# Optimization experiments

Hardware: AMD Instinct MI355X
Metric: run time of the kernel (lower is better)

Reference implementation:

```python
import jax, jax.numpy as jnp
import numpy as np

B, T, C = 4, 2048, 768
NH, NKV, HD = 12, 12, 64
RMS_EPS = 1e-6


def rms_norm(x):
    return x * jax.lax.rsqrt(jnp.mean(x * x, axis=-1, keepdims=True) + RMS_EPS)


def apply_rotary_emb(x, cos, sin):
    # x: [B,T,H,D], cos/sin: [T,D/2]
    d2 = x.shape[-1] // 2
    x1, x2 = x[..., :d2], x[..., d2:]
    c = cos[None, :, None, :]
    s = sin[None, :, None, :]
    return jnp.concatenate([x1 * c - x2 * s, x1 * s + x2 * c], axis=-1)


def setup_inputs() -> dict:
    key = jax.random.key(0)
    ks = jax.random.split(key, 10)
    inv_freq = 1.0 / (100000.0 ** (np.arange(0, HD, 2, dtype=np.float32) / HD))  # [HD/2]
    t = np.arange(T, dtype=np.float32)
    freqs = np.outer(t, inv_freq)  # [T, HD/2]
    return {
        "x": jax.random.normal(ks[0], (B, T, C), jnp.float32),
        "ve": jax.random.normal(ks[1], (B, T, C), jnp.float32),
        "cos": jnp.asarray(np.cos(freqs)),
        "sin": jnp.asarray(np.sin(freqs)),
        "Wq": jax.random.normal(ks[2], (C, C), jnp.float32) * (1.0 / np.sqrt(C)),
        "Wk": jax.random.normal(ks[3], (C, C), jnp.float32) * (1.0 / np.sqrt(C)),
        "Wv": jax.random.normal(ks[4], (C, C), jnp.float32) * (1.0 / np.sqrt(C)),
        "Wproj": jax.random.normal(ks[5], (C, C), jnp.float32) * (1.0 / np.sqrt(C)),
        "Wgate": jax.random.normal(ks[6], (NKV, 12), jnp.float32) * 0.1,
        "window_left": 1024,
    }


def reference(x, ve, cos, sin, Wq, Wk, Wv, Wproj, Wgate, window_left):
    q = (x @ Wq.T).reshape(B, T, NH, HD)
    k = (x @ Wk.T).reshape(B, T, NKV, HD)
    v = (x @ Wv.T).reshape(B, T, NKV, HD)

    # value-embedding gating (has_ve path): gate = 3*sigmoid(Linear(x[...,:12]))
    ve_h = ve.reshape(B, T, NKV, HD)
    gate = 3.0 * jax.nn.sigmoid(x[..., :12] @ Wgate.T)  # [B,T,NKV]
    v = v + gate[..., None] * ve_h

    q = apply_rotary_emb(q, cos, sin)
    k = apply_rotary_emb(k, cos, sin)
    q = rms_norm(q) * 1.2
    k = rms_norm(k) * 1.2

    # sliding-window causal bias
    row = jnp.arange(T)[:, None]
    col = jnp.arange(T)[None, :]
    mask = (row >= col) & ((row - col) <= window_left)
    bias = jnp.where(mask, 0.0, -1e9).astype(x.dtype)  # [T,T]

    scale = 1.0 / np.sqrt(HD)
    att = jnp.einsum("bqhd,bkhd->bhqk", q, k) * scale + bias[None, None]
    att = jax.nn.softmax(att, axis=-1)
    y = jnp.einsum("bhqk,bkhd->bqhd", att, v).reshape(B, T, C)
    return y @ Wproj.T
```

## Files before the change

### kernel.cpp

```cpp
#include <hip/hip_runtime.h>
#include <hip/hip_bf16.h>
#include <cstdint>
#include <cstddef>

#define B_  4
#define T_  2048
#define C_  768
#define NH_ 12
#define HD_ 64

typedef __bf16 bf16_t;
typedef __attribute__((ext_vector_type(8))) __bf16 bf16x8;
typedef __attribute__((ext_vector_type(4))) __bf16 bf16x4;
typedef __attribute__((ext_vector_type(4))) float floatx4;
typedef __attribute__((ext_vector_type(8))) unsigned short ushort8;

#define MFMA16(a, b, c) __builtin_amdgcn_mfma_f32_16x16x32_bf16((a), (b), (c), 0, 0, 0)

#define SM_C1 0.18033688f
#define SM_C2 -17.3123405f

typedef const __attribute__((address_space(1))) uint8_t* gptr_t;
typedef __attribute__((address_space(3))) uint8_t* lptr_t;

static __device__ __forceinline__ void gld16(const void* g, void* l) {
    __builtin_amdgcn_global_load_lds((gptr_t)g, (lptr_t)l, 16, 0, 0);
}

static __device__ __forceinline__ float bfl(unsigned p) {
    return __builtin_bit_cast(float, p << 16);
}
static __device__ __forceinline__ float bfh(unsigned p) {
    return __builtin_bit_cast(float, p & 0xffff0000u);
}

__global__ __launch_bounds__(256) void cvt_all_kernel(
    const void* s0, const void* s1, const void* s2, const void* s3,
    const void* s4, const void* s5, const void* s6, const void* s7, const void* s8,
    bf16_t* d0, bf16_t* d1, bf16_t* d2, bf16_t* d3,
    bf16_t* d4, bf16_t* d5, bf16_t* d6, bf16_t* d7, bf16_t* d8)
{
    const bool isf32 = (((const unsigned short*)s2)[0] == 0);
    if (!isf32) return;
    const void* srcs[9] = {s0, s1, s2, s3, s4, s5, s6, s7, s8};
    bf16_t*     dsts[9] = {d0, d1, d2, d3, d4, d5, d6, d7, d8};
    const int   ns[9]   = {B_*T_*C_, B_*T_*C_, T_*32, T_*32,
                           C_*C_, C_*C_, C_*C_, C_*C_, 144};
    const int t = blockIdx.y;
    const float* sf = (const float*)srcs[t];
    bf16_t*     dst = dsts[t];
    const int   nc  = ns[t] >> 3;
    const int stride = gridDim.x * 256;
    for (int i = blockIdx.x * 256 + threadIdx.x; i < nc; i += stride) {
        ushort8 o;
#pragma unroll
        for (int j = 0; j < 8; j++)
            o[j] = (unsigned short)__builtin_bit_cast(unsigned short,
                     (bf16_t)sf[i * 8 + j]);
        *(ushort8*)&dst[i * 8] = o;
    }
}

__global__ __launch_bounds__(256) void gemm_qkv_fused(
    const void* xr,  const bf16_t* xc,
    const void* wqr, const bf16_t* wqc,
    const void* wkr, const bf16_t* wkc,
    const void* wvr, const bf16_t* wvc,
    const void* cr,  const bf16_t* ccv,
    const void* sr,  const bf16_t* scv,
    const void* ver, const bf16_t* vec,
    const void* wgr, const bf16_t* wgc,
    bf16_t* qn, bf16_t* kn, bf16_t* vt)
{
    __shared__ alignas(16) char sm[36864];
    const bool f32 = (((const unsigned short*)cr)[0] == 0);
    const bf16_t* X  = f32 ? xc  : (const bf16_t*)xr;
    const bf16_t* WQ = f32 ? wqc : (const bf16_t*)wqr;
    const bf16_t* WK = f32 ? wkc : (const bf16_t*)wkr;
    const bf16_t* WV = f32 ? wvc : (const bf16_t*)wvr;
    const bf16_t* CC = f32 ? ccv : (const bf16_t*)cr;
    const bf16_t* SS = f32 ? scv : (const bf16_t*)sr;
    const bf16_t* VE = f32 ? vec : (const bf16_t*)ver;
    const bf16_t* WG = f32 ? wgc : (const bf16_t*)wgr;

    const int sel = blockIdx.y / 6;
    const int nt  = blockIdx.y % 6;
    const int m0  = blockIdx.x * 128;
    const int n0  = nt * 128;
    const bf16_t* Bm = (sel == 0) ? WQ : (sel == 1) ? WK : WV;

    bf16_t* As = (bf16_t*)sm;
    bf16_t* Bs = (bf16_t*)(sm + 16384);

    const int tid  = threadIdx.x;
    const int lane = tid & 63;
    const int wid  = tid >> 6;
    const int m16  = lane & 15;
    const int quad = lane >> 4;
    const int wm   = (wid >> 1) * 64;
    const int wn   = (wid & 1) * 64;
    const int srow = lane >> 2;
    const int soct = (lane & 3) * 8;

    floatx4 acc[4][4];
#pragma unroll
    for (int i = 0; i < 4; i++)
#pragma unroll
        for (int j = 0; j < 4; j++) acc[i][j] = (floatx4){0.f, 0.f, 0.f, 0.f};

    for (int k0 = 0; k0 < C_; k0 += 64) {
        const bf16_t* ga0 = &X[(size_t)(m0 + 16 * wid + srow) * C_ + k0 + soct];
        const bf16_t* gb0 = &Bm[(size_t)(n0 + 16 * wid + srow) * C_ + k0 + soct];
        gld16(ga0,                        As + wid * 512);
        gld16(ga0 + (size_t)64 * C_,      As + wid * 512 + 2048);
        gld16(gb0,                        Bs + wid * 512);
        gld16(gb0 + (size_t)64 * C_,      Bs + wid * 512 + 2048);
        gld16(ga0 + 32,                   As + 4096 + wid * 512);
        gld16(ga0 + (size_t)64 * C_ + 32, As + 4096 + wid * 512 + 2048);
        gld16(gb0 + 32,                   Bs + 4096 + wid * 512);
        gld16(gb0 + (size_t)64 * C_ + 32, Bs + 4096 + wid * 512 + 2048);
        __syncthreads();
#pragma unroll
        for (int half = 0; half < 2; half++) {
            bf16x8 af[4], bfr[4];
#pragma unroll
            for (int i = 0; i < 4; i++)
                af[i] = *(const bf16x8*)&As[half * 4096 + (wm + i * 16 + m16) * 32 + quad * 8];
#pragma unroll
            for (int j = 0; j < 4; j++)
                bfr[j] = *(const bf16x8*)&Bs[half * 4096 + (wn + j * 16 + m16) * 32 + quad * 8];
#pragma unroll
            for (int i = 0; i < 4; i++)
#pragma unroll
                for (int j = 0; j < 4; j++)
                    acc[i][j] = MFMA16(af[i], bfr[j], acc[i][j]);
        }
        __syncthreads();
    }

    if (sel < 2) {
        unsigned* csT = (unsigned*)sm;
        const int tbase = m0 & 2047;
        for (int idx = tid; idx < 128 * 32; idx += 256) {
            const int rr = idx >> 5, dd = idx & 31;
            const unsigned cv = ((const unsigned short*)CC)[(tbase + rr) * 32 + dd];
            const unsigned sv = ((const unsigned short*)SS)[(tbase + rr) * 32 + dd];
            csT[rr * 33 + dd] = cv | (sv << 16);
        }
        __syncthreads();
        bf16_t* OUT = (sel == 0) ? qn : kn;
#pragma unroll
        for (int i = 0; i < 4; i++) {
            float c0[4], s0[4], c1[4], s1[4];
#pragma unroll
            for (int r = 0; r < 4; r++) {
                const int rl = wm + i * 16 + quad * 4 + r;
                const unsigned p0 = csT[rl * 33 + m16];
                const unsigned p1 = csT[rl * 33 + 16 + m16];
                c0[r] = bfl(p0); s0[r] = bfh(p0);
                c1[r] = bfl(p1); s1[r] = bfh(p1);
            }
            floatx4 r0, r1, r2, r3;
            float ss[4];
#pragma unroll
            for (int r = 0; r < 4; r++) {
                r0[r] = acc[i][0][r] * c0[r] - acc[i][2][r] * s0[r];
                r1[r] = acc[i][1][r] * c1[r] - acc[i][3][r] * s1[r];
                r2[r] = acc[i][0][r] * s0[r] + acc[i][2][r] * c0[r];
                r3[r] = acc[i][1][r] * s1[r] + acc[i][3][r] * c1[r];
                ss[r] = r0[r]*r0[r] + r1[r]*r1[r] + r2[r]*r2[r] + r3[r]*r3[r];
            }
#pragma unroll
            for (int r = 0; r < 4; r++) {
#pragma unroll
                for (int off = 1; off < 16; off <<= 1)
                    ss[r] += __shfl_xor(ss[r], off, 64);
            }
#pragma unroll
            for (int r = 0; r < 4; r++) {
                const float scl = rsqrtf(ss[r] * (1.f / 64.f) + 1e-6f) * 1.2f;
                const size_t rowoff = (size_t)(m0 + wm + i * 16 + quad * 4 + r) * C_
                                      + n0 + wn + m16;
                OUT[rowoff]      = (bf16_t)(r0[r] * scl);
                OUT[rowoff + 16] = (bf16_t)(r1[r] * scl);
                OUT[rowoff + 32] = (bf16_t)(r2[r] * scl);
                OUT[rowoff + 48] = (bf16_t)(r3[r] * scl);
            }
        }
    } else {
        bf16_t* veT = (bf16_t*)sm;
        float*  gT  = (float*)(sm + 34816);
        for (int idx = tid; idx < 2048; idx += 256) {
            const int rr = idx >> 4, ch = idx & 15;
            *(bf16x8*)&veT[rr * 136 + ch * 8] =
                *(const bf16x8*)&VE[(size_t)(m0 + rr) * C_ + n0 + ch * 8];
        }
        {
            const int row = tid & 127, hh = tid >> 7;
            const int head = nt * 2 + hh;
            float g = 0.f;
#pragma unroll
            for (int j2 = 0; j2 < 12; j2++)
                g += (float)X[(size_t)(m0 + row) * C_ + j2] * (float)WG[head * 12 + j2];
            gT[hh * 128 + row] = 3.f / (1.f + __expf(-g));
        }
        __syncthreads();
        const int hh2  = wn >> 6;
        const int head = nt * 2 + hh2;
        const int bb = m0 >> 11, t0 = m0 & 2047;
#pragma unroll
        for (int i = 0; i < 4; i++) {
            const floatx4 gr = *(const floatx4*)&gT[hh2 * 128 + wm + i * 16 + quad * 4];
            const int tslot = t0 + wm + (i >> 1) * 32 + quad * 8 + (i & 1) * 4;
#pragma unroll
            for (int j = 0; j < 4; j++) {
                bf16x4 o;
#pragma unroll
                for (int r = 0; r < 4; r++) {
                    const float vef = (float)veT[(wm + i * 16 + quad * 4 + r) * 136
                                                 + wn + j * 16 + m16];
                    o[r] = (bf16_t)(acc[i][j][r] + gr[r] * vef);
                }
                *(bf16x4*)&vt[((size_t)(bb * NH_ + head) * HD_ + j * 16 + m16) * T_
                              + tslot] = o;
            }
        }
    }
}

template <bool OUT_BF16>
__device__ __forceinline__ void gemm_bt_tile(
    const bf16_t* __restrict__ A, const bf16_t* __restrict__ Bm,
    void* __restrict__ Cout, int m0, int n0, int K, int ldc)
{
    __shared__ bf16_t As[2][128 * 32];
    __shared__ bf16_t Bs[2][128 * 32];
    const int tid  = threadIdx.x;
    const int lane = tid & 63;
    const int wid  = tid >> 6;
    const int m16  = lane & 15;
    const int quad = lane >> 4;
    const int wm   = (wid >> 1) * 64;
    const int wn   = (wid & 1) * 64;
    const int srow = lane >> 2;
    const int soct = (lane & 3) * 8;

    floatx4 acc[4][4];
#pragma unroll
    for (int i = 0; i < 4; i++)
#pragma unroll
        for (int j = 0; j < 4; j++) acc[i][j] = (floatx4){0.f, 0.f, 0.f, 0.f};

    for (int k0 = 0; k0 < K; k0 += 64) {
        const bf16_t* ga0 = &A[(size_t)(m0 + 16 * wid + srow) * K + k0 + soct];
        const bf16_t* gb0 = &Bm[(size_t)(n0 + 16 * wid + srow) * K + k0 + soct];
        gld16(ga0,                       (bf16_t*)As[0] + wid * 512);
        gld16(ga0 + (size_t)64 * K,      (bf16_t*)As[0] + wid * 512 + 2048);
        gld16(gb0,                       (bf16_t*)Bs[0] + wid * 512);
        gld16(gb0 + (size_t)64 * K,      (bf16_t*)Bs[0] + wid * 512 + 2048);
        gld16(ga0 + 32,                  (bf16_t*)As[1] + wid * 512);
        gld16(ga0 + (size_t)64 * K + 32, (bf16_t*)As[1] + wid * 512 + 2048);
        gld16(gb0 + 32,                  (bf16_t*)Bs[1] + wid * 512);
        gld16(gb0 + (size_t)64 * K + 32, (bf16_t*)Bs[1] + wid * 512 + 2048);
        __syncthreads();
#pragma unroll
        for (int half = 0; half < 2; half++) {
            bf16x8 af[4], bfr[4];
#pragma unroll
            for (int i = 0; i < 4; i++)
                af[i] = *(const bf16x8*)&As[half][(wm + i * 16 + m16) * 32 + quad * 8];
#pragma unroll
            for (int j = 0; j < 4; j++)
                bfr[j] = *(const bf16x8*)&Bs[half][(wn + j * 16 + m16) * 32 + quad * 8];
#pragma unroll
            for (int i = 0; i < 4; i++)
#pragma unroll
                for (int j = 0; j < 4; j++)
                    acc[i][j] = MFMA16(af[i], bfr[j], acc[i][j]);
        }
        __syncthreads();
    }
#pragma unroll
    for (int i = 0; i < 4; i++) {
#pragma unroll
        for (int j = 0; j < 4; j++) {
            const int colg = n0 + wn + j * 16 + m16;
#pragma unroll
            for (int r = 0; r < 4; r++) {
                const int rowg = m0 + wm + i * 16 + quad * 4 + r;
                if (OUT_BF16)
                    ((bf16_t*)Cout)[(size_t)rowg * ldc + colg] = (bf16_t)acc[i][j][r];
                else
                    ((float*)Cout)[(size_t)rowg * ldc + colg] = acc[i][j][r];
            }
        }
    }
}

__global__ __launch_bounds__(256) void gemm_proj_kernel(
    const bf16_t* __restrict__ yb, const void* wpr, const bf16_t* wpc,
    void* __restrict__ out, const void* cr)
{
    const bool f32 = (((const unsigned short*)cr)[0] == 0);
    const bf16_t* WP = f32 ? wpc : (const bf16_t*)wpr;
    if (f32)
        gemm_bt_tile<false>(yb, WP, out, blockIdx.x * 128, blockIdx.y * 128, C_, C_);
    else
        gemm_bt_tile<true>(yb, WP, out, blockIdx.x * 128, blockIdx.y * 128, C_, C_);
}

__global__ __launch_bounds__(256, 3) void attn_kernel(
    const bf16_t* __restrict__ Q, const bf16_t* __restrict__ Km,
    const bf16_t* __restrict__ Vtg, bf16_t* __restrict__ Y,
    const int* __restrict__ wl)
{
    const int bx   = blockIdx.x;
    const int bh   = blockIdx.y;
    const int gsel = bh >> 4;
    int qblk;
    if (gsel == 0)      qblk = bx;
    else if (gsel == 1) qblk = 15 - bx;
    else                qblk = (int)((0xECA8642013579BDFull >> (bx * 4)) & 0xF);
    const int q0 = qblk * 128;
    const int b  = bh / NH_;
    const int h  = bh % NH_;
    const int window = wl[0];
    const int tid  = threadIdx.x;
    const int wid  = tid >> 6;
    const int lane = tid & 63;
    const int m16  = lane & 15;
    const int quad = lane >> 4;
    const int qw   = q0 + wid * 32;

    const bf16_t* Qb = Q + (size_t)b * T_ * C_ + h * HD_;
    const bf16_t* Kb = Km + (size_t)b * T_ * C_ + h * HD_;
    const bf16_t* Vb = Vtg + (size_t)bh * HD_ * T_;

    __shared__ bf16_t Ks[2][64 * 64];
    __shared__ bf16_t Vs[2][64 * 64];

    bf16x8 qf[2][2];
#pragma unroll
    for (int mt = 0; mt < 2; mt++)
#pragma unroll
        for (int ks = 0; ks < 2; ks++)
            qf[mt][ks] = *(const bf16x8*)
                &Qb[(size_t)(qw + mt * 16 + m16) * C_ + ks * 32 + quad * 8];

    const int srow = tid >> 2;
    const int soct = tid & 3;
    const int g0   = 2 * soct, g1 = 2 * soct + 1;
    const int kd0  = srow * 64 + ((g0 ^ (srow & 7)) << 3);
    const int kd1  = srow * 64 + ((g1 ^ (srow & 7)) << 3);
    int rsw[2];
#pragma unroll
    for (int ks = 0; ks < 2; ks++)
        rsw[ks] = (((ks * 4 + quad) ^ (m16 & 7)) << 3);

    int lo = q0 - window;
    if (lo < 0) lo = 0;
    lo &= ~63;
    const int nch = (q0 + 128 - lo) >> 6;

    floatx4 accO[2][4];
#pragma unroll
    for (int mt = 0; mt < 2; mt++)
#pragma unroll
        for (int dt = 0; dt < 4; dt++) accO[mt][dt] = (floatx4){0.f, 0.f, 0.f, 0.f};
    float lsum[2] = {0.f, 0.f};
    const bf16x4 zero4 = {(bf16_t)0.f, (bf16_t)0.f, (bf16_t)0.f, (bf16_t)0.f};

    bf16x8 ka0 = *(const bf16x8*)&Kb[(size_t)(lo + srow) * C_ + g0 * 8];
    bf16x8 ka1 = *(const bf16x8*)&Kb[(size_t)(lo + srow) * C_ + g1 * 8];
    bf16x8 va0 = *(const bf16x8*)&Vb[(size_t)srow * T_ + lo + g0 * 8];
    bf16x8 va1 = *(const bf16x8*)&Vb[(size_t)srow * T_ + lo + g1 * 8];
    *(bf16x8*)&Ks[0][kd0] = ka0;
    *(bf16x8*)&Ks[0][kd1] = ka1;
    *(bf16x8*)&Vs[0][kd0] = va0;
    *(bf16x8*)&Vs[0][kd1] = va1;

    for (int ic = 0; ic < nch; ic++) {
        const int kc = lo + ic * 64;
        const bool more = (ic + 1 < nch);
        if (more) {
            const int kn2 = kc + 64;
            ka0 = *(const bf16x8*)&Kb[(size_t)(kn2 + srow) * C_ + g0 * 8];
            ka1 = *(const bf16x8*)&Kb[(size_t)(kn2 + srow) * C_ + g1 * 8];
            va0 = *(const bf16x8*)&Vb[(size_t)srow * T_ + kn2 + g0 * 8];
            va1 = *(const bf16x8*)&Vb[(size_t)srow * T_ + kn2 + g1 * 8];
        }
        __syncthreads();
        const int buf = ic & 1;

        const bool skip = (kc > qw + 31) || (kc + 63 < qw - window);
        if (!skip) {
            bf16x8 kf[4][2];
#pragma unroll
            for (int nt = 0; nt < 4; nt++) {
                const int rb = (nt * 16 + m16) * 64;
                kf[nt][0] = *(const bf16x8*)&Ks[buf][rb + rsw[0]];
                kf[nt][1] = *(const bf16x8*)&Ks[buf][rb + rsw[1]];
            }
            bf16x4 pk[2][4];
            unsigned livemask = 0;
#pragma unroll
            for (int mt = 0; mt < 2; mt++) {
                const int qmin = qw + mt * 16, qmax = qmin + 15;
                float lacc = 0.f;
#pragma unroll
                for (int nt = 0; nt < 4; nt++) {
                    const int kmin = kc + nt * 16, kmax = kmin + 15;
                    if (kmin > qmax || kmax < qmin - window) {
                        pk[mt][nt] = zero4;
                        continue;
                    }
                    livemask |= 1u << (mt * 4 + nt);
                    floatx4 z = (floatx4){0.f, 0.f, 0.f, 0.f};
                    z = MFMA16(kf[nt][0], qf[mt][0], z);
                    z = MFMA16(kf[nt][1], qf[mt][1], z);
                    const bool edge = (kmax > qmin) || (kmin < qmax - window);
                    const int query = qmin + m16;
                    bf16x4 t4;
#pragma unroll
                    for (int r = 0; r < 4; r++) {
                        float p = __builtin_amdgcn_exp2f(
                            fmaf(z[r], SM_C1, SM_C2));
                        if (edge) {
                            const int key = kmin + quad * 4 + r;
                            const bool ok = (key <= query) &&
                                            (query - key <= window);
                            p = ok ? p : 0.f;
                        }
                        t4[r] = (bf16_t)p;
                        lacc += p;
                    }
                    pk[mt][nt] = t4;
                }
                lsum[mt] += lacc;
            }
#pragma unroll
            for (int pr = 0; pr < 2; pr++) {
                const unsigned pm0 = (livemask >> (2 * pr)) & 3u;
                const unsigned pm1 = (livemask >> (4 + 2 * pr)) & 3u;
                if (!(pm0 | pm1)) continue;
                const bf16x8 pa0 = __builtin_shufflevector(
                    pk[0][2 * pr], pk[0][2 * pr + 1], 0, 1, 2, 3, 4, 5, 6, 7);
                const bf16x8 pa1 = __builtin_shufflevector(
                    pk[1][2 * pr], pk[1][2 * pr + 1], 0, 1, 2, 3, 4, 5, 6, 7);
                const int vco = (((pr * 4 + quad) ^ (m16 & 7)) << 3);
#pragma unroll
                for (int dt = 0; dt < 4; dt++) {
                    const bf16x8 vf = *(const bf16x8*)
                        &Vs[buf][(dt * 16 + m16) * 64 + vco];
                    if (pm0) accO[0][dt] = MFMA16(pa0, vf, accO[0][dt]);
                    if (pm1) accO[1][dt] = MFMA16(pa1, vf, accO[1][dt]);
                }
            }
        }

        if (more) {
            const int nb = buf ^ 1;
            *(bf16x8*)&Ks[nb][kd0] = ka0;
            *(bf16x8*)&Ks[nb][kd1] = ka1;
            *(bf16x8*)&Vs[nb][kd0] = va0;
            *(bf16x8*)&Vs[nb][kd1] = va1;
        }
    }

#pragma unroll
    for (int mt = 0; mt < 2; mt++) {
        float red = lsum[mt];
        red += __shfl_xor(red, 16, 64);
        red += __shfl_xor(red, 32, 64);
#pragma unroll
        for (int r = 0; r < 4; r++) {
            const float lq  = __shfl(red, quad * 4 + r, 64);
            const float inv = 1.f / lq;
            const int   tq  = qw + mt * 16 + quad * 4 + r;
#pragma unroll
            for (int dt = 0; dt < 4; dt++)
                Y[((size_t)b * T_ + tq) * C_ + h * HD_ + dt * 16 + m16] =
                    (bf16_t)(accO[mt][dt][r] * inv);
        }
    }
}

extern "C" void kernel_launch(void* const* d_in, const int* in_sizes, int n_in,
                              void* d_out, int out_size, void* d_ws, size_t ws_size,
                              hipStream_t stream)
{
    const void* x_raw   = d_in[0];
    const void* ve_raw  = d_in[1];
    const void* cos_raw = d_in[2];
    const void* sin_raw = d_in[3];
    const void* wq_raw  = d_in[4];
    const void* wk_raw  = d_in[5];
    const void* wv_raw  = d_in[6];
    const void* wp_raw  = d_in[7];
    const void* wg_raw  = d_in[8];
    const int*  wl      = (const int*)d_in[9];

    const size_t NTC = (size_t)B_ * T_ * C_;
    const size_t WSZ = (size_t)C_ * C_;

    bf16_t* ws  = (bf16_t*)d_ws;
    bf16_t* xb  = ws;
    bf16_t* veb = xb + NTC;
    bf16_t* cb  = veb + NTC;
    bf16_t* sb  = cb + T_ * 32;
    bf16_t* wqb = sb + T_ * 32;
    bf16_t* wkb = wqb + WSZ;
    bf16_t* wvb = wkb + WSZ;
    bf16_t* wpb = wvb + WSZ;
    bf16_t* wgb = wpb + WSZ;
    bf16_t* qn  = wgb + 256;
    bf16_t* kn  = qn + NTC;
    bf16_t* vt  = kn + NTC;
    bf16_t* yb  = vt + NTC;

    cvt_all_kernel<<<dim3(128, 9), 256, 0, stream>>>(
        x_raw, ve_raw, cos_raw, sin_raw, wq_raw, wk_raw, wv_raw, wp_raw, wg_raw,
        xb, veb, cb, sb, wqb, wkb, wvb, wpb, wgb);

    gemm_qkv_fused<<<dim3(64, 18), 256, 0, stream>>>(
        x_raw, xb, wq_raw, wqb, wk_raw, wkb, wv_raw, wvb,
        cos_raw, cb, sin_raw, sb, ve_raw, veb, wg_raw, wgb,
        qn, kn, vt);

    attn_kernel<<<dim3(16, 48), 256, 0, stream>>>(qn, kn, vt, yb, wl);

    gemm_proj_kernel<<<dim3(64, 6), 256, 0, stream>>>(yb, wp_raw, wpb, d_out, cos_raw);
}
```

Baseline: 249.8 us.

## Rewrite QKV GEMM as 256x256 tile with double-buffered, 8-wave pipelined mainloop

The fused QKV projection kernel now uses 512-thread blocks computing 256x256 output tiles with 128KB of LDS. Global-to-LDS loads for the next K tiles are double-buffered and interleaved with four MFMA phases, with raised wave priority around the MFMAs and an XOR swizzle on LDS columns. The aim is to overlap memory loads with matrix math and raise arithmetic intensity per loaded byte. In exchange, the grid shrinks to 288 blocks at one block per CU, the value-embedding add now reads VE straight from global memory instead of staging it in LDS, and register pressure rises.

```diff
diff --git a/kernel.cpp b/kernel.cpp
--- a/kernel.cpp
+++ b/kernel.cpp
@@ -61,7 +61,7 @@
     }
 }
 
-__global__ __launch_bounds__(256) void gemm_qkv_fused(
+__global__ __launch_bounds__(512) void gemm_qkv_fused(
     const void* xr,  const bf16_t* xc,
     const void* wqr, const bf16_t* wqc,
     const void* wkr, const bf16_t* wkc,
@@ -72,7 +72,7 @@
     const void* wgr, const bf16_t* wgc,
     bf16_t* qn, bf16_t* kn, bf16_t* vt)
 {
-    __shared__ alignas(16) char sm[36864];
+    __shared__ alignas(16) char sm[131072];
     const bool f32 = (((const unsigned short*)cr)[0] == 0);
     const bf16_t* X  = f32 ? xc  : (const bf16_t*)xr;
     const bf16_t* WQ = f32 ? wqc : (const bf16_t*)wqr;
@@ -83,65 +83,145 @@
     const bf16_t* VE = f32 ? vec : (const bf16_t*)ver;
     const bf16_t* WG = f32 ? wgc : (const bf16_t*)wgr;
 
-    const int sel = blockIdx.y / 6;
-    const int nt  = blockIdx.y % 6;
-    const int m0  = blockIdx.x * 128;
-    const int n0  = nt * 128;
+    const int tileN = blockIdx.y;
+    const int sel   = tileN / 3;
+    const int m0    = blockIdx.x * 256;
+    const int brow0 = (tileN % 3) * 256;
     const bf16_t* Bm = (sel == 0) ? WQ : (sel == 1) ? WK : WV;
-
-    bf16_t* As = (bf16_t*)sm;
-    bf16_t* Bs = (bf16_t*)(sm + 16384);
 
     const int tid  = threadIdx.x;
     const int lane = tid & 63;
     const int wid  = tid >> 6;
+    const int wr   = wid >> 2;
+    const int wc   = wid & 3;
     const int m16  = lane & 15;
     const int quad = lane >> 4;
-    const int wm   = (wid >> 1) * 64;
-    const int wn   = (wid & 1) * 64;
-    const int srow = lane >> 2;
-    const int soct = (lane & 3) * 8;
-
-    floatx4 acc[4][4];
-#pragma unroll
-    for (int i = 0; i < 4; i++)
+    const int qb   = (quad * 16) ^ ((m16 & 4) ? 32 : 0);
+
+    const int s_r  = tid >> 3;
+    const int s_ce = ((tid & 7) * 8) ^ ((tid & 32) ? 16 : 0);
+    char* const wdst = sm + (size_t)(tid & ~63) * 16;
+
+#define STA(d, h, kt) do {                                                   \
+        char* _dst = wdst + ((d) * 2 + (h)) * 16384;                         \
+        const bf16_t* _g = &X[(size_t)(m0 + (h) * 128 + s_r) * C_            \
+                              + (kt) * 64 + s_ce];                           \
+        gld16(_g, _dst);                                                     \
+        gld16(_g + (size_t)64 * C_, _dst + 8192);                            \
+    } while (0)
+#define STB(d, h, kt) do {                                                   \
+        char* _dst = wdst + 65536 + ((d) * 2 + (h)) * 16384;                 \
+        const bf16_t* _g = &Bm[(size_t)(brow0 + (h) * 128 + s_r) * C_        \
+                               + (kt) * 64 + s_ce];                          \
+        gld16(_g, _dst);                                                     \
+        gld16(_g + (size_t)64 * C_, _dst + 8192);                            \
+    } while (0)
+
+    floatx4 acc[8][4];
+#pragma unroll
+    for (int i = 0; i < 8; i++)
 #pragma unroll
         for (int j = 0; j < 4; j++) acc[i][j] = (floatx4){0.f, 0.f, 0.f, 0.f};
 
-    for (int k0 = 0; k0 < C_; k0 += 64) {
-        const bf16_t* ga0 = &X[(size_t)(m0 + 16 * wid + srow) * C_ + k0 + soct];
-        const bf16_t* gb0 = &Bm[(size_t)(n0 + 16 * wid + srow) * C_ + k0 + soct];
-        gld16(ga0,                        As + wid * 512);
-        gld16(ga0 + (size_t)64 * C_,      As + wid * 512 + 2048);
-        gld16(gb0,                        Bs + wid * 512);
-        gld16(gb0 + (size_t)64 * C_,      Bs + wid * 512 + 2048);
-        gld16(ga0 + 32,                   As + 4096 + wid * 512);
-        gld16(ga0 + (size_t)64 * C_ + 32, As + 4096 + wid * 512 + 2048);
-        gld16(gb0 + 32,                   Bs + 4096 + wid * 512);
-        gld16(gb0 + (size_t)64 * C_ + 32, Bs + 4096 + wid * 512 + 2048);
-        __syncthreads();
-#pragma unroll
-        for (int half = 0; half < 2; half++) {
-            bf16x8 af[4], bfr[4];
-#pragma unroll
-            for (int i = 0; i < 4; i++)
-                af[i] = *(const bf16x8*)&As[half * 4096 + (wm + i * 16 + m16) * 32 + quad * 8];
-#pragma unroll
-            for (int j = 0; j < 4; j++)
-                bfr[j] = *(const bf16x8*)&Bs[half * 4096 + (wn + j * 16 + m16) * 32 + quad * 8];
-#pragma unroll
-            for (int i = 0; i < 4; i++)
-#pragma unroll
-                for (int j = 0; j < 4; j++)
-                    acc[i][j] = MFMA16(af[i], bfr[j], acc[i][j]);
-        }
-        __syncthreads();
+    const int NT = C_ / 64;
+
+    STB(0, 0, 0); STA(0, 0, 0); STB(0, 1, 0); STA(0, 1, 0);
+    STB(1, 0, 1); STA(1, 0, 1);
+    asm volatile("s_waitcnt vmcnt(4)" ::: "memory");
+    __builtin_amdgcn_s_barrier();
+
+    for (int t = 0; t < NT; t++) {
+        const int d   = t & 1;
+        const int tp1 = (t + 1 == NT) ? 0 : t + 1;
+        const int tp2 = (t + 2 >= NT) ? (t + 2 - NT) : t + 2;
+        const char* Ah = sm + (d * 2 + wr) * 16384;
+        const char* Bh = sm + 65536 + (d * 2 + (wc >> 1)) * 16384;
+        const int brow = (wc & 1) * 64;
+
+        bf16x8 afA[4][2], bfA[2][2], bfB[2][2], afB[4][2];
+
+#pragma unroll
+        for (int i = 0; i < 4; i++)
+#pragma unroll
+            for (int ks = 0; ks < 2; ks++)
+                afA[i][ks] = *(const bf16x8*)(Ah + (i * 16 + m16) * 128 + ks * 64 + qb);
+#pragma unroll
+        for (int j = 0; j < 2; j++)
+#pragma unroll
+            for (int ks = 0; ks < 2; ks++)
+                bfA[j][ks] = *(const bf16x8*)(Bh + (brow + j * 16 + m16) * 128 + ks * 64 + qb);
+        STB(d ^ 1, 1, tp1);
+        __builtin_amdgcn_s_barrier();
+        __builtin_amdgcn_s_setprio(1);
+#pragma unroll
+        for (int i = 0; i < 4; i++)
+#pragma unroll
+            for (int j = 0; j < 2; j++)
+#pragma unroll
+                for (int ks = 0; ks < 2; ks++)
+                    acc[i][j] = MFMA16(afA[i][ks], bfA[j][ks], acc[i][j]);
+        __builtin_amdgcn_s_setprio(0);
+        __builtin_amdgcn_s_barrier();
+
+#pragma unroll
+        for (int j = 0; j < 2; j++)
+#pragma unroll
+            for (int ks = 0; ks < 2; ks++)
+                bfB[j][ks] = *(const bf16x8*)(Bh + (brow + (j + 2) * 16 + m16) * 128 + ks * 64 + qb);
+        STA(d ^ 1, 1, tp1);
+        __builtin_amdgcn_s_barrier();
+        __builtin_amdgcn_s_setprio(1);
+#pragma unroll
+        for (int i = 0; i < 4; i++)
+#pragma unroll
+            for (int j = 0; j < 2; j++)
+#pragma unroll
+                for (int ks = 0; ks < 2; ks++)
+                    acc[i][j + 2] = MFMA16(afA[i][ks], bfB[j][ks], acc[i][j + 2]);
+        __builtin_amdgcn_s_setprio(0);
+        __builtin_amdgcn_s_barrier();
+
+#pragma unroll
+        for (int i = 0; i < 4; i++)
+#pragma unroll
+            for (int ks = 0; ks < 2; ks++)
+                afB[i][ks] = *(const bf16x8*)(Ah + ((i + 4) * 16 + m16) * 128 + ks * 64 + qb);
+        STB(d, 0, tp2);
+        __builtin_amdgcn_s_barrier();
+        __builtin_amdgcn_s_setprio(1);
+#pragma unroll
+        for (int i = 0; i < 4; i++)
+#pragma unroll
+            for (int j = 0; j < 2; j++)
+#pragma unroll
+                for (int ks = 0; ks < 2; ks++)
+                    acc[i + 4][j + 2] = MFMA16(afB[i][ks], bfB[j][ks], acc[i + 4][j + 2]);
+        __builtin_amdgcn_s_setprio(0);
+        __builtin_amdgcn_s_barrier();
+
+        STA(d, 0, tp2);
+        __builtin_amdgcn_s_barrier();
+        __builtin_amdgcn_s_setprio(1);
+#pragma unroll
+        for (int i = 0; i < 4; i++)
+#pragma unroll
+            for (int j = 0; j < 2; j++)
+#pragma unroll
+                for (int ks = 0; ks < 2; ks++)
+                    acc[i + 4][j] = MFMA16(afB[i][ks], bfA[j][ks], acc[i + 4][j]);
+        __builtin_amdgcn_s_setprio(0);
+        asm volatile("s_waitcnt vmcnt(4)" ::: "memory");
+        __builtin_amdgcn_s_barrier();
     }
+#undef STA
+#undef STB
+
+    __syncthreads();
 
     if (sel < 2) {
         unsigned* csT = (unsigned*)sm;
         const int tbase = m0 & 2047;
-        for (int idx = tid; idx < 128 * 32; idx += 256) {
+        for (int idx = tid; idx < 256 * 32; idx += 512) {
             const int rr = idx >> 5, dd = idx & 31;
             const unsigned cv = ((const unsigned short*)CC)[(tbase + rr) * 32 + dd];
             const unsigned sv = ((const unsigned short*)SS)[(tbase + rr) * 32 + dd];
@@ -149,12 +229,13 @@
         }
         __syncthreads();
         bf16_t* OUT = (sel == 0) ? qn : kn;
-#pragma unroll
-        for (int i = 0; i < 4; i++) {
+        const int colb = brow0 + wc * 64;
+#pragma unroll
+        for (int i = 0; i < 8; i++) {
             float c0[4], s0[4], c1[4], s1[4];
 #pragma unroll
             for (int r = 0; r < 4; r++) {
-                const int rl = wm + i * 16 + quad * 4 + r;
+                const int rl = wr * 128 + i * 16 + quad * 4 + r;
                 const unsigned p0 = csT[rl * 33 + m16];
                 const unsigned p1 = csT[rl * 33 + 16 + m16];
                 c0[r] = bfl(p0); s0[r] = bfh(p0);
@@ -179,8 +260,8 @@
 #pragma unroll
             for (int r = 0; r < 4; r++) {
                 const float scl = rsqrtf(ss[r] * (1.f / 64.f) + 1e-6f) * 1.2f;
-                const size_t rowoff = (size_t)(m0 + wm + i * 16 + quad * 4 + r) * C_
-                                      + n0 + wn + m16;
+                const size_t rowoff = (size_t)(m0 + wr * 128 + i * 16 + quad * 4 + r) * C_
+                                      + colb + m16;
                 OUT[rowoff]      = (bf16_t)(r0[r] * scl);
                 OUT[rowoff + 16] = (bf16_t)(r1[r] * scl);
                 OUT[rowoff + 32] = (bf16_t)(r2[r] * scl);
@@ -188,37 +269,32 @@
             }
         }
     } else {
-        bf16_t* veT = (bf16_t*)sm;
-        float*  gT  = (float*)(sm + 34816);
-        for (int idx = tid; idx < 2048; idx += 256) {
-            const int rr = idx >> 4, ch = idx & 15;
-            *(bf16x8*)&veT[rr * 136 + ch * 8] =
-                *(const bf16x8*)&VE[(size_t)(m0 + rr) * C_ + n0 + ch * 8];
-        }
-        {
-            const int row = tid & 127, hh = tid >> 7;
-            const int head = nt * 2 + hh;
+        float* gT = (float*)sm;
+        const int headb = (tileN - 6) * 4;
+        for (int task = tid; task < 1024; task += 512) {
+            const int hh = task >> 8, row = task & 255;
             float g = 0.f;
 #pragma unroll
             for (int j2 = 0; j2 < 12; j2++)
-                g += (float)X[(size_t)(m0 + row) * C_ + j2] * (float)WG[head * 12 + j2];
-            gT[hh * 128 + row] = 3.f / (1.f + __expf(-g));
+                g += (float)X[(size_t)(m0 + row) * C_ + j2]
+                   * (float)WG[(headb + hh) * 12 + j2];
+            gT[hh * 256 + row] = 3.f / (1.f + __expf(-g));
         }
         __syncthreads();
-        const int hh2  = wn >> 6;
-        const int head = nt * 2 + hh2;
+        const int head = headb + wc;
         const int bb = m0 >> 11, t0 = m0 & 2047;
 #pragma unroll
-        for (int i = 0; i < 4; i++) {
-            const floatx4 gr = *(const floatx4*)&gT[hh2 * 128 + wm + i * 16 + quad * 4];
-            const int tslot = t0 + wm + (i >> 1) * 32 + quad * 8 + (i & 1) * 4;
+        for (int i = 0; i < 8; i++) {
+            const floatx4 gr = *(const floatx4*)&gT[wc * 256 + wr * 128 + i * 16 + quad * 4];
+            const int tslot = t0 + wr * 128 + (i >> 2) * 64
+                              + ((i >> 1) & 1) * 32 + quad * 8 + (i & 1) * 4;
 #pragma unroll
             for (int j = 0; j < 4; j++) {
                 bf16x4 o;
 #pragma unroll
                 for (int r = 0; r < 4; r++) {
-                    const float vef = (float)veT[(wm + i * 16 + quad * 4 + r) * 136
-                                                 + wn + j * 16 + m16];
+                    const float vef = (float)VE[(size_t)(m0 + wr * 128 + i * 16 + quad * 4 + r) * C_
+                                                + head * 64 + j * 16 + m16];
                     o[r] = (bf16_t)(acc[i][j][r] + gr[r] * vef);
                 }
                 *(bf16x4*)&vt[((size_t)(bb * NH_ + head) * HD_ + j * 16 + m16) * T_
@@ -522,7 +598,7 @@
         x_raw, ve_raw, cos_raw, sin_raw, wq_raw, wk_raw, wv_raw, wp_raw, wg_raw,
         xb, veb, cb, sb, wqb, wkb, wvb, wpb, wgb);
 
-    gemm_qkv_fused<<<dim3(64, 18), 256, 0, stream>>>(
+    gemm_qkv_fused<<<dim3(32, 9), 512, 0, stream>>>(
         x_raw, xb, wq_raw, wqb, wk_raw, wkb, wv_raw, wvb,
         cos_raw, cb, sin_raw, sb, ve_raw, veb, wg_raw, wgb,
         qn, kn, vt);
```

After: 258.1 us. 1.03x slower.
